# Kernel tuning notes

Measured on AMD Instinct MI355X. Metric: run time of the kernel, lower is better.

The kernel has to match this reference:

```python
import jax, jax.numpy as jnp
import numpy as np

H_KV = 8          # num_key_value_heads (hard-coded in module)
N_HEADS = 32
HEAD_DIM = 128
GROUPS = N_HEADS // H_KV
EPS = 1e-05
ROPE_THETA = 10000.0


def rotate_half(x):
    x1, x2 = jnp.split(x, 2, axis=-1)
    return jnp.concatenate((-x2, x1), axis=-1)


def rms_norm(x, w, eps=EPS):
    xf = x.astype(jnp.float32)
    var = jnp.mean(xf * xf, axis=-1, keepdims=True)
    return (w * (xf * jax.lax.rsqrt(var + eps))).astype(x.dtype)


def setup_inputs() -> dict:
    key = jax.random.key(0)
    k1, k2, k3 = jax.random.split(key, 3)
    B, S, D = 2, 2048, 4096
    hidden_states = jax.random.normal(k1, (B, S, D), dtype=jnp.float32)
    # RoPE tables (what custom_pos_emb carries)
    inv_freq = 1.0 / (ROPE_THETA ** (jnp.arange(0, HEAD_DIM, 2, dtype=jnp.float32) / HEAD_DIM))
    t = jnp.arange(S, dtype=jnp.float32)
    freqs = jnp.outer(t, inv_freq)                 # [S, HEAD_DIM/2]
    emb = jnp.concatenate((freqs, freqs), axis=-1)  # [S, HEAD_DIM]
    cos = jnp.cos(emb)[None]                        # [1, S, HEAD_DIM]
    sin = jnp.sin(emb)[None]
    w_qkv = jax.random.normal(k2, (6144, D), dtype=jnp.float32) * 0.02
    w_o = jax.random.normal(k3, (D, D), dtype=jnp.float32) * 0.02
    q_norm_w = jnp.ones((HEAD_DIM,), dtype=jnp.float32)
    k_norm_w = jnp.ones((HEAD_DIM,), dtype=jnp.float32)
    return {"hidden_states": hidden_states, "cos": cos, "sin": sin,
            "w_qkv": w_qkv, "w_o": w_o, "q_norm_w": q_norm_w, "k_norm_w": k_norm_w}


def reference(hidden_states, cos, sin, w_qkv, w_o, q_norm_w, k_norm_w):
    B, S, D = hidden_states.shape
    qkv = hidden_states @ w_qkv.T                                    # [B,S,6144]
    qkv = qkv.reshape(B, S, H_KV, GROUPS + 2, HEAD_DIM)
    q = qkv[:, :, :, :GROUPS]                                        # [B,S,Hkv,G,d]
    k = qkv[:, :, :, GROUPS]                                         # [B,S,Hkv,d]
    v = qkv[:, :, :, GROUPS + 1]                                     # [B,S,Hkv,d]
    # to [B, heads, S, d]
    q = q.reshape(B, S, N_HEADS, HEAD_DIM).transpose(0, 2, 1, 3)     # [B,Hq,S,d]
    k = k.transpose(0, 2, 1, 3)                                      # [B,Hkv,S,d]
    v = v.transpose(0, 2, 1, 3)
    # RoPE (cos/sin: [1,S,d] -> unsqueeze head dim)
    c = cos[:, None]  # [1,1,S,d]
    s = sin[:, None]
    q = q * c + rotate_half(q) * s
    k = k * c + rotate_half(k) * s
    # per-head RMSNorm
    q = rms_norm(q, q_norm_w)
    k = rms_norm(k, k_norm_w)
    # GQA attention without materializing repeated K/V
    qg = q.reshape(B, H_KV, GROUPS, S, HEAD_DIM)
    scale = 1.0 / np.sqrt(HEAD_DIM).astype(np.float32)
    scores = jnp.einsum('bkgqd,bksd->bkgqs', qg, k) * scale          # [B,Hkv,G,S,S]
    probs = jax.nn.softmax(scores, axis=-1)
    out = jnp.einsum('bkgqs,bksd->bkgqd', probs, v)                  # [B,Hkv,G,S,d]
    out = out.reshape(B, N_HEADS, S, HEAD_DIM).transpose(0, 2, 1, 3).reshape(B, S, D)
    return out @ w_o.T
```

## Files before the change

### kernel.cpp

```cpp
#include <hip/hip_runtime.h>
#include <hip/hip_bf16.h>

typedef __attribute__((ext_vector_type(8))) short short8;
typedef __attribute__((ext_vector_type(4))) float floatx4;

static __device__ __forceinline__ short bf16bits(float f) {
    __hip_bfloat16 h = __float2bfloat16(f);
    return __builtin_bit_cast(short, h);
}

#define GLDS(g, l) __builtin_amdgcn_global_load_lds( \
    (const __attribute__((address_space(1))) void*)(g), \
    (__attribute__((address_space(3))) void*)(l), 16, 0, 0)

__global__ __launch_bounds__(256) void cvt_bf16(
    const float* __restrict__ src, __hip_bfloat16* __restrict__ dst)
{
    size_t i = ((size_t)blockIdx.x * 256 + threadIdx.x) * 8;
    floatx4 f0 = *(const floatx4*)(src + i);
    floatx4 f1 = *(const floatx4*)(src + i + 4);
    short8 s;
#pragma unroll
    for (int j = 0; j < 4; j++) { s[j] = bf16bits(f0[j]); s[j + 4] = bf16bits(f1[j]); }
    *(short8*)((short*)dst + i) = s;
}

template<typename CT>
__global__ __launch_bounds__(256) void gemm_bt_fast(
    const __hip_bfloat16* __restrict__ A,
    const __hip_bfloat16* __restrict__ W,
    CT* __restrict__ C, int M, int N, int K)
{
    __shared__ alignas(16) short lA[128 * 64];
    __shared__ alignas(16) short lB[128 * 64];

    const int tid  = threadIdx.x;
    const int wave = tid >> 6;
    const int lane = tid & 63;
    const int quad = lane >> 4;
    const int l16  = lane & 15;

    const int m0 = blockIdx.x * 128;
    const int n0 = blockIdx.y * 128;
    const int wm = (wave & 1) * 64;
    const int wn = (wave >> 1) * 64;

    const int srow = lane >> 3;
    const int sblk = (lane & 7) ^ srow;
    const int scol = sblk * 8;

    const short* Ag = (const short*)A;
    const short* Wg = (const short*)W;

    floatx4 acc[4][4];
#pragma unroll
    for (int i = 0; i < 4; i++)
#pragma unroll
        for (int j = 0; j < 4; j++) acc[i][j] = (floatx4)0.0f;

    for (int k0 = 0; k0 < K; k0 += 64) {
        __syncthreads();
#pragma unroll
        for (int i = 0; i < 4; i++) {
            int c   = wave * 4 + i;
            int row = c * 8 + srow;
            GLDS(Ag + (size_t)(m0 + row) * K + k0 + scol, &lA[c * 512]);
            GLDS(Wg + (size_t)(n0 + row) * K + k0 + scol, &lB[c * 512]);
        }
        __syncthreads();
#pragma unroll
        for (int kk2 = 0; kk2 < 2; kk2++) {
            const int pb = ((kk2 * 4 + quad) ^ (l16 & 7)) * 8;
            short8 af[4], bf[4];
#pragma unroll
            for (int i = 0; i < 4; i++)
                af[i] = *(const short8*)(&lA[(wm + i * 16 + l16) * 64 + pb]);
#pragma unroll
            for (int j = 0; j < 4; j++)
                bf[j] = *(const short8*)(&lB[(wn + j * 16 + l16) * 64 + pb]);
#pragma unroll
            for (int i = 0; i < 4; i++)
#pragma unroll
                for (int j = 0; j < 4; j++)
                    acc[i][j] = __builtin_amdgcn_mfma_f32_16x16x32_bf16(
                        af[i], bf[j], acc[i][j], 0, 0, 0);
        }
    }
#pragma unroll
    for (int i = 0; i < 4; i++)
#pragma unroll
        for (int j = 0; j < 4; j++) {
            int gm = m0 + wm + i * 16 + quad * 4;
            int gn = n0 + wn + j * 16 + l16;
#pragma unroll
            for (int r = 0; r < 4; r++) {
                float v = acc[i][j][r];
                if constexpr (sizeof(CT) == 2)
                    C[(size_t)(gm + r) * N + gn] = (CT)__float2bfloat16(v);
                else
                    C[(size_t)(gm + r) * N + gn] = (CT)v;
            }
        }
}

template<bool AF32, typename CT>
__global__ __launch_bounds__(256) void gemm_bt_slow(
    const void* __restrict__ A,
    const float* __restrict__ Wf,
    CT* __restrict__ C, int M, int N, int K)
{
    __shared__ alignas(16) short lA[128 * 72];
    __shared__ alignas(16) short lB[128 * 72];

    const int tid  = threadIdx.x;
    const int wave = tid >> 6;
    const int lane = tid & 63;
    const int quad = lane >> 4;
    const int l16  = lane & 15;

    const int m0 = blockIdx.x * 128;
    const int n0 = blockIdx.y * 128;
    const int wm = (wave & 1) * 64;
    const int wn = (wave >> 1) * 64;

    floatx4 acc[4][4];
#pragma unroll
    for (int i = 0; i < 4; i++)
#pragma unroll
        for (int j = 0; j < 4; j++) acc[i][j] = (floatx4)0.0f;

    const short* Ab = (const short*)A;
    const float* Af = (const float*)A;

    for (int k0 = 0; k0 < K; k0 += 64) {
        __syncthreads();
#pragma unroll
        for (int i = 0; i < 4; i++) {
            int chunk = tid + i * 256;
            int row = chunk >> 3;
            int cc  = chunk & 7;
            if (AF32) {
                const float* src = Af + (size_t)(m0 + row) * K + k0 + cc * 8;
                floatx4 f0 = *(const floatx4*)(src);
                floatx4 f1 = *(const floatx4*)(src + 4);
                short8 s;
#pragma unroll
                for (int j = 0; j < 4; j++) { s[j] = bf16bits(f0[j]); s[j + 4] = bf16bits(f1[j]); }
                *(short8*)(&lA[row * 72 + cc * 8]) = s;
            } else {
                *(short8*)(&lA[row * 72 + cc * 8]) =
                    *(const short8*)(Ab + (size_t)(m0 + row) * K + k0 + cc * 8);
            }
            const float* src = Wf + (size_t)(n0 + row) * K + k0 + cc * 8;
            floatx4 f0 = *(const floatx4*)(src);
            floatx4 f1 = *(const floatx4*)(src + 4);
            short8 s;
#pragma unroll
            for (int j = 0; j < 4; j++) { s[j] = bf16bits(f0[j]); s[j + 4] = bf16bits(f1[j]); }
            *(short8*)(&lB[row * 72 + cc * 8]) = s;
        }
        __syncthreads();
#pragma unroll
        for (int kk = 0; kk < 64; kk += 32) {
            short8 af[4], bf[4];
#pragma unroll
            for (int i = 0; i < 4; i++)
                af[i] = *(const short8*)(&lA[(wm + i * 16 + l16) * 72 + kk + quad * 8]);
#pragma unroll
            for (int j = 0; j < 4; j++)
                bf[j] = *(const short8*)(&lB[(wn + j * 16 + l16) * 72 + kk + quad * 8]);
#pragma unroll
            for (int i = 0; i < 4; i++)
#pragma unroll
                for (int j = 0; j < 4; j++)
                    acc[i][j] = __builtin_amdgcn_mfma_f32_16x16x32_bf16(
                        af[i], bf[j], acc[i][j], 0, 0, 0);
        }
    }
#pragma unroll
    for (int i = 0; i < 4; i++)
#pragma unroll
        for (int j = 0; j < 4; j++) {
            int gm = m0 + wm + i * 16 + quad * 4;
            int gn = n0 + wn + j * 16 + l16;
#pragma unroll
            for (int r = 0; r < 4; r++) {
                float v = acc[i][j][r];
                if constexpr (sizeof(CT) == 2)
                    C[(size_t)(gm + r) * N + gn] = (CT)__float2bfloat16(v);
                else
                    C[(size_t)(gm + r) * N + gn] = (CT)v;
            }
        }
}

__global__ __launch_bounds__(256) void rope_norm(
    __hip_bfloat16* __restrict__ qkv,
    const float* __restrict__ cosb,
    const float* __restrict__ sinb,
    const float* __restrict__ qw,
    const float* __restrict__ kw)
{
    int wid  = blockIdx.x * 4 + (threadIdx.x >> 6);
    int lane = threadIdx.x & 63;
    int token = wid / 40;
    int idx   = wid % 40;
    int s = token & 2047;

    int off;
    const float* w;
    if (idx < 32) { off = (idx >> 2) * 768 + (idx & 3) * 128; w = qw; }
    else          { off = (idx - 32) * 768 + 512;             w = kw; }

    short* p = (short*)(qkv + (size_t)token * 6144 + off);
    int d = lane * 2;

    unsigned int pv = *(const unsigned int*)(p + d);
    float x0 = __builtin_bit_cast(float, pv << 16);
    float x1 = __builtin_bit_cast(float, pv & 0xffff0000u);

    float ox0 = __shfl_xor(x0, 32, 64);
    float ox1 = __shfl_xor(x1, 32, 64);

    float2 cv = *(const float2*)(cosb + s * 128 + d);
    float2 sv = *(const float2*)(sinb + s * 128 + d);
    float sgn = (lane < 32) ? -1.0f : 1.0f;
    float y0 = fmaf(sgn * ox0, sv.x, x0 * cv.x);
    float y1 = fmaf(sgn * ox1, sv.y, x1 * cv.y);

    float ss = y0 * y0 + y1 * y1;
#pragma unroll
    for (int m = 1; m < 64; m <<= 1) ss += __shfl_xor(ss, m, 64);
    float r = rsqrtf(ss * (1.0f / 128.0f) + 1e-5f);

    float2 wv = *(const float2*)(w + d);
    unsigned int out = (unsigned int)(unsigned short)bf16bits(y0 * r * wv.x)
                     | ((unsigned int)(unsigned short)bf16bits(y1 * r * wv.y) << 16);
    *(unsigned int*)(p + d) = out;
}

__global__ __launch_bounds__(256) void vtrans(
    const __hip_bfloat16* __restrict__ qkv, __hip_bfloat16* __restrict__ Vt)
{
    __shared__ alignas(16) short lT[64 * 136];

    const int bid   = blockIdx.x;
    const int stile = bid & 31;
    const int kvh   = (bid >> 5) & 7;
    const int b     = bid >> 8;
    const int tid   = threadIdx.x;
    const size_t voff = (size_t)kvh * 768 + 640;
    const short* qkvs = (const short*)qkv;

#pragma unroll
    for (int i = 0; i < 4; i++) {
        int chunk = tid + i * 256;
        int t  = chunk >> 4;
        int dc = chunk & 15;
        size_t tok = (size_t)(b * 2048 + stile * 64 + t);
        *(short8*)(&lT[t * 136 + dc * 8]) =
            *(const short8*)(qkvs + tok * 6144 + voff + dc * 8);
    }
    __syncthreads();

    int d  = tid >> 1;
    int kh = (tid & 1) * 32;
    short* out = (short*)Vt + ((size_t)((b * 8 + kvh) * 128 + d)) * 2048
               + stile * 64 + kh;
#pragma unroll
    for (int jb = 0; jb < 4; jb++) {
        short8 s;
#pragma unroll
        for (int j = 0; j < 8; j++) s[j] = lT[(kh + jb * 8 + j) * 136 + d];
        *(short8*)(out + jb * 8) = s;
    }
}

__global__ __launch_bounds__(256, 2) void attn_kernel(
    const __hip_bfloat16* __restrict__ qkv,
    const __hip_bfloat16* __restrict__ Vt,
    __hip_bfloat16* __restrict__ attn_out)
{
    __shared__ alignas(16) short lK[2][64 * 128];
    __shared__ alignas(16) short lVt[2][128 * 64];
    __shared__ alignas(16) short lP[4][32 * 64];

    const int bid0 = blockIdx.x;
    const int bid  = (bid0 & 7) * 128 + (bid0 >> 3);
    const int qt   = bid & 15;
    const int h    = (bid >> 4) & 31;
    const int b    = bid >> 9;
    const int kvh  = h >> 2;
    const int wave = threadIdx.x >> 6;
    const int lane = threadIdx.x & 63;
    const int quad = lane >> 4;
    const int l16  = lane & 15;

    const size_t qoff = (size_t)kvh * 768 + (size_t)(h & 3) * 128;
    const size_t koff = (size_t)kvh * 768 + 512;
    const short* qkvs = (const short*)qkv;
    const short* Vts  = (const short*)Vt + ((size_t)(b * 8 + kvh) * 128) * 2048;

    short8 qf[2][4];
#pragma unroll
    for (int t = 0; t < 2; t++) {
        const int qrow = qt * 128 + wave * 32 + t * 16 + l16;
        const size_t qtok = (size_t)(b * 2048 + qrow);
#pragma unroll
        for (int kk = 0; kk < 4; kk++)
            qf[t][kk] = *(const short8*)(qkvs + qtok * 6144 + qoff + kk * 32 + quad * 8);
    }

    floatx4 o[2][8];
#pragma unroll
    for (int t = 0; t < 2; t++)
#pragma unroll
        for (int n = 0; n < 8; n++) o[t][n] = (floatx4)0.0f;
    float mrow[2][4], lsum[2][4];
#pragma unroll
    for (int t = 0; t < 2; t++)
#pragma unroll
        for (int r = 0; r < 4; r++) { mrow[t][r] = -3.0e4f; lsum[t][r] = 0.0f; }

    const float scale2 = 0.08838834764831845f * 1.4426950408889634f;
    const float THR2   = 11.5418f;

    const int k_row = lane >> 4;
    const int v_row = lane >> 3;
    const int v_blk = (lane & 7) ^ v_row;

#pragma unroll
    for (int i = 0; i < 4; i++) {
        int c = wave * 4 + i;
        int k_blk = (lane & 15) ^ ((c * 4 + k_row) & 15);
        size_t tok = (size_t)(b * 2048 + c * 4 + k_row);
        GLDS(qkvs + tok * 6144 + koff + k_blk * 8, &lK[0][c * 512]);
        int d = c * 8 + v_row;
        GLDS(Vts + (size_t)d * 2048 + v_blk * 8, &lVt[0][c * 512]);
    }

    int cur = 0;
    for (int kt = 0; kt < 32; kt++) {
        __syncthreads();

        if (kt < 31) {
            short* nK = &lK[cur ^ 1][0];
            short* nV = &lVt[cur ^ 1][0];
#pragma unroll
            for (int i = 0; i < 4; i++) {
                int c = wave * 4 + i;
                int k_blk = (lane & 15) ^ ((c * 4 + k_row) & 15);
                size_t tok = (size_t)(b * 2048 + (kt + 1) * 64 + c * 4 + k_row);
                GLDS(qkvs + tok * 6144 + koff + k_blk * 8, nK + c * 512);
                int d = c * 8 + v_row;
                GLDS(Vts + (size_t)d * 2048 + (kt + 1) * 64 + v_blk * 8, nV + c * 512);
            }
        }

        const short* lKc = &lK[cur][0];
        const short* lVc = &lVt[cur][0];

        floatx4 sc[2][4];
#pragma unroll
        for (int t = 0; t < 2; t++)
#pragma unroll
            for (int n = 0; n < 4; n++) sc[t][n] = (floatx4)0.0f;
#pragma unroll
        for (int kk = 0; kk < 4; kk++) {
#pragma unroll
            for (int n = 0; n < 4; n++) {
                short8 bfr = *(const short8*)(
                    &lKc[(n * 16 + l16) * 128 + (((kk * 4 + quad) ^ l16)) * 8]);
                sc[0][n] = __builtin_amdgcn_mfma_f32_16x16x32_bf16(qf[0][kk], bfr, sc[0][n], 0, 0, 0);
                sc[1][n] = __builtin_amdgcn_mfma_f32_16x16x32_bf16(qf[1][kk], bfr, sc[1][n], 0, 0, 0);
            }
        }

#pragma unroll
        for (int t = 0; t < 2; t++) {
            float mx[4]; int grow = 0;
#pragma unroll
            for (int r = 0; r < 4; r++) {
                float m0 = fmaxf(fmaxf(sc[t][0][r], sc[t][1][r]),
                                 fmaxf(sc[t][2][r], sc[t][3][r])) * scale2;
#pragma unroll
                for (int m = 1; m < 16; m <<= 1) m0 = fmaxf(m0, __shfl_xor(m0, m, 64));
                mx[r] = m0;
                grow |= (m0 > mrow[t][r] + THR2) ? 1 : 0;
            }
            const bool big = __any(grow) != 0;
            float alpha[4];
            if (big) {
#pragma unroll
                for (int r = 0; r < 4; r++) {
                    float mn = fmaxf(mrow[t][r], mx[r]);
                    alpha[r] = exp2f(mrow[t][r] - mn);
                    mrow[t][r] = mn;
                }
            }
#pragma unroll
            for (int n = 0; n < 4; n++)
#pragma unroll
                for (int r = 0; r < 4; r++) {
                    float p = exp2f(sc[t][n][r] * scale2 - mrow[t][r]);
                    sc[t][n][r] = p;
                    int row = t * 16 + quad * 4 + r;
                    int pblk = (n * 2 + (l16 >> 3)) ^ (row & 7);
                    lP[wave][row * 64 + pblk * 8 + (l16 & 7)] = bf16bits(p);
                }
#pragma unroll
            for (int r = 0; r < 4; r++) {
                float ps = (sc[t][0][r] + sc[t][1][r]) + (sc[t][2][r] + sc[t][3][r]);
                if (big) lsum[t][r] = lsum[t][r] * alpha[r] + ps;
                else     lsum[t][r] += ps;
            }
            if (big) {
#pragma unroll
                for (int n = 0; n < 8; n++)
#pragma unroll
                    for (int r = 0; r < 4; r++) o[t][n][r] *= alpha[r];
            }
        }

        __threadfence_block();

#pragma unroll
        for (int kk2 = 0; kk2 < 2; kk2++) {
            const int pb = ((kk2 * 4 + quad) ^ (l16 & 7)) * 8;
            short8 pf0 = *(const short8*)(&lP[wave][(l16)      * 64 + pb]);
            short8 pf1 = *(const short8*)(&lP[wave][(16 + l16) * 64 + pb]);
#pragma unroll
            for (int n = 0; n < 8; n++) {
                short8 vf = *(const short8*)(&lVc[(n * 16 + l16) * 64 + pb]);
                o[0][n] = __builtin_amdgcn_mfma_f32_16x16x32_bf16(pf0, vf, o[0][n], 0, 0, 0);
                o[1][n] = __builtin_amdgcn_mfma_f32_16x16x32_bf16(pf1, vf, o[1][n], 0, 0, 0);
            }
        }

        cur ^= 1;
    }

#pragma unroll
    for (int t = 0; t < 2; t++)
#pragma unroll
        for (int r = 0; r < 4; r++) {
            float s = lsum[t][r];
#pragma unroll
            for (int m = 1; m < 16; m <<= 1) s += __shfl_xor(s, m, 64);
            lsum[t][r] = 1.0f / s;
        }

#pragma unroll
    for (int t = 0; t < 2; t++)
#pragma unroll
        for (int n = 0; n < 8; n++)
#pragma unroll
            for (int r = 0; r < 4; r++) {
                int row = qt * 128 + wave * 32 + t * 16 + quad * 4 + r;
                size_t tok = (size_t)(b * 2048 + row);
                attn_out[tok * 4096 + h * 128 + n * 16 + l16] =
                    __float2bfloat16(o[t][n][r] * lsum[t][r]);
            }
}

extern "C" void kernel_launch(void* const* d_in, const int* in_sizes, int n_in,
                              void* d_out, int out_size, void* d_ws, size_t ws_size,
                              hipStream_t stream) {
    const float* hidden = (const float*)d_in[0];
    const float* cosb   = (const float*)d_in[1];
    const float* sinb   = (const float*)d_in[2];
    const float* w_qkv  = (const float*)d_in[3];
    const float* w_o    = (const float*)d_in[4];
    const float* qw     = (const float*)d_in[5];
    const float* kw     = (const float*)d_in[6];

    char* ws = (char*)d_ws;
    __hip_bfloat16* qkv    = (__hip_bfloat16*)ws;
    __hip_bfloat16* attn_o = (__hip_bfloat16*)(ws + 50331648);
    __hip_bfloat16* hb  = (__hip_bfloat16*)(ws + 83886080);
    __hip_bfloat16* wb1 = (__hip_bfloat16*)(ws + 117440512);
    __hip_bfloat16* wb2 = (__hip_bfloat16*)(ws + 167772160);
    const size_t WS_FAST = 201326592;

    __hip_bfloat16* Vt = (__hip_bfloat16*)d_out;
    float* outp        = (float*)d_out;

    const bool fast = (ws_size >= WS_FAST);

    if (fast) {
        cvt_bf16<<<16777216 / 8 / 256, 256, 0, stream>>>(hidden, hb);
        cvt_bf16<<<25165824 / 8 / 256, 256, 0, stream>>>(w_qkv, wb1);
        cvt_bf16<<<16777216 / 8 / 256, 256, 0, stream>>>(w_o, wb2);
        dim3 g1(32, 48);
        gemm_bt_fast<__hip_bfloat16><<<g1, 256, 0, stream>>>(hb, wb1, qkv, 4096, 6144, 4096);
    } else {
        dim3 g1(32, 48);
        gemm_bt_slow<true, __hip_bfloat16><<<g1, 256, 0, stream>>>(hidden, w_qkv, qkv, 4096, 6144, 4096);
    }

    rope_norm<<<40960, 256, 0, stream>>>(qkv, cosb, sinb, qw, kw);

    vtrans<<<512, 256, 0, stream>>>(qkv, Vt);

    attn_kernel<<<1024, 256, 0, stream>>>(qkv, Vt, attn_o);

    dim3 g2(32, 32);
    if (fast) {
        gemm_bt_fast<float><<<g2, 256, 0, stream>>>(attn_o, wb2, outp, 4096, 4096, 4096);
    } else {
        gemm_bt_slow<false, float><<<g2, 256, 0, stream>>>(attn_o, w_o, outp, 4096, 4096, 4096);
    }
}
```

Measured before the change: 894.2 us.

## Compute transposed S in attention to keep P in registers instead of LDS

Swaps the MFMA operands so each lane holds scores for one query row across keys. Row max and sum then need only two cross-lane shuffles, and the online-softmax state shrinks to one value per tile. Probabilities are packed to bf16 with v_cvt_pk_bf16_f32 and rearranged with lane shuffles into the PV operand layout, removing the per-wave LDS buffer, its scalar stores and the block fence. Output stores become 4-element vector writes. The cost is extra ds_bpermute shuffles and selects, plus inline asm that depends on the ISA providing that instruction.

New measurement: 875.7 us. 1.02x faster.

```diff
diff --git a/kernel.cpp b/kernel.cpp
--- a/kernel.cpp
+++ b/kernel.cpp
@@ -2,11 +2,19 @@
 #include <hip/hip_bf16.h>
 
 typedef __attribute__((ext_vector_type(8))) short short8;
+typedef __attribute__((ext_vector_type(4))) short short4v;
 typedef __attribute__((ext_vector_type(4))) float floatx4;
+typedef __attribute__((ext_vector_type(4))) unsigned int uintx4;
 
 static __device__ __forceinline__ short bf16bits(float f) {
     __hip_bfloat16 h = __float2bfloat16(f);
     return __builtin_bit_cast(short, h);
+}
+
+static __device__ __forceinline__ unsigned int cvtpk(float lo, float hi) {
+    unsigned int r;
+    asm("v_cvt_pk_bf16_f32 %0, %1, %2" : "=v"(r) : "v"(lo), "v"(hi));
+    return r;
 }
 
 #define GLDS(g, l) __builtin_amdgcn_global_load_lds( \
@@ -283,7 +291,6 @@
 {
     __shared__ alignas(16) short lK[2][64 * 128];
     __shared__ alignas(16) short lVt[2][128 * 64];
-    __shared__ alignas(16) short lP[4][32 * 64];
 
     const int bid0 = blockIdx.x;
     const int bid  = (bid0 & 7) * 128 + (bid0 >> 3);
@@ -291,8 +298,8 @@
     const int h    = (bid >> 4) & 31;
     const int b    = bid >> 9;
     const int kvh  = h >> 2;
+    const int lane = threadIdx.x & 63;
     const int wave = threadIdx.x >> 6;
-    const int lane = threadIdx.x & 63;
     const int quad = lane >> 4;
     const int l16  = lane & 15;
 
@@ -316,11 +323,8 @@
     for (int t = 0; t < 2; t++)
 #pragma unroll
         for (int n = 0; n < 8; n++) o[t][n] = (floatx4)0.0f;
-    float mrow[2][4], lsum[2][4];
-#pragma unroll
-    for (int t = 0; t < 2; t++)
-#pragma unroll
-        for (int r = 0; r < 4; r++) { mrow[t][r] = -3.0e4f; lsum[t][r] = 0.0f; }
+    float mrow[2] = { -3.0e4f, -3.0e4f };
+    float lsum[2] = { 0.0f, 0.0f };
 
     const float scale2 = 0.08838834764831845f * 1.4426950408889634f;
     const float THR2   = 11.5418f;
@@ -328,6 +332,10 @@
     const int k_row = lane >> 4;
     const int v_row = lane >> 3;
     const int v_blk = (lane & 7) ^ v_row;
+
+    const int srcA = l16 + ((lane & 16) << 1);
+    const int srcB = srcA + 16;
+    const bool hi2 = (quad >> 1) != 0;
 
 #pragma unroll
     for (int i = 0; i < 4; i++) {
@@ -369,98 +377,108 @@
         for (int kk = 0; kk < 4; kk++) {
 #pragma unroll
             for (int n = 0; n < 4; n++) {
-                short8 bfr = *(const short8*)(
+                short8 kf = *(const short8*)(
                     &lKc[(n * 16 + l16) * 128 + (((kk * 4 + quad) ^ l16)) * 8]);
-                sc[0][n] = __builtin_amdgcn_mfma_f32_16x16x32_bf16(qf[0][kk], bfr, sc[0][n], 0, 0, 0);
-                sc[1][n] = __builtin_amdgcn_mfma_f32_16x16x32_bf16(qf[1][kk], bfr, sc[1][n], 0, 0, 0);
-            }
-        }
-
+                sc[0][n] = __builtin_amdgcn_mfma_f32_16x16x32_bf16(kf, qf[0][kk], sc[0][n], 0, 0, 0);
+                sc[1][n] = __builtin_amdgcn_mfma_f32_16x16x32_bf16(kf, qf[1][kk], sc[1][n], 0, 0, 0);
+            }
+        }
+
+        short8 pb[2][2];
 #pragma unroll
         for (int t = 0; t < 2; t++) {
-            float mx[4]; int grow = 0;
-#pragma unroll
-            for (int r = 0; r < 4; r++) {
-                float m0 = fmaxf(fmaxf(sc[t][0][r], sc[t][1][r]),
-                                 fmaxf(sc[t][2][r], sc[t][3][r])) * scale2;
-#pragma unroll
-                for (int m = 1; m < 16; m <<= 1) m0 = fmaxf(m0, __shfl_xor(m0, m, 64));
-                mx[r] = m0;
-                grow |= (m0 > mrow[t][r] + THR2) ? 1 : 0;
-            }
-            const bool big = __any(grow) != 0;
-            float alpha[4];
-            if (big) {
+            float ma = fmaxf(fmaxf(sc[t][0][0], sc[t][0][1]), fmaxf(sc[t][0][2], sc[t][0][3]));
+            float mb = fmaxf(fmaxf(sc[t][1][0], sc[t][1][1]), fmaxf(sc[t][1][2], sc[t][1][3]));
+            float mc = fmaxf(fmaxf(sc[t][2][0], sc[t][2][1]), fmaxf(sc[t][2][2], sc[t][2][3]));
+            float md = fmaxf(fmaxf(sc[t][3][0], sc[t][3][1]), fmaxf(sc[t][3][2], sc[t][3][3]));
+            float mr = fmaxf(fmaxf(ma, mb), fmaxf(mc, md));
+            mr = fmaxf(mr, __shfl_xor(mr, 16, 64));
+            mr = fmaxf(mr, __shfl_xor(mr, 32, 64));
+            float mx = mr * scale2;
+
+            int grown = mx > mrow[t] + THR2;
+            if (__any(grown)) {
+                float mn = fmaxf(mrow[t], mx);
+                float alpha = exp2f(mrow[t] - mn);
+                mrow[t] = mn;
+                lsum[t] *= alpha;
+#pragma unroll
+                for (int n = 0; n < 8; n++)
+#pragma unroll
+                    for (int r = 0; r < 4; r++) o[t][n][r] *= alpha;
+            }
+
+            const float nm = -mrow[t];
+            float ps = 0.0f;
+            unsigned int pk[4][2];
+#pragma unroll
+            for (int n = 0; n < 4; n++) {
 #pragma unroll
                 for (int r = 0; r < 4; r++) {
-                    float mn = fmaxf(mrow[t][r], mx[r]);
-                    alpha[r] = exp2f(mrow[t][r] - mn);
-                    mrow[t][r] = mn;
+                    float pv = exp2f(fmaf(sc[t][n][r], scale2, nm));
+                    sc[t][n][r] = pv;
+                    ps += pv;
                 }
-            }
-#pragma unroll
-            for (int n = 0; n < 4; n++)
-#pragma unroll
-                for (int r = 0; r < 4; r++) {
-                    float p = exp2f(sc[t][n][r] * scale2 - mrow[t][r]);
-                    sc[t][n][r] = p;
-                    int row = t * 16 + quad * 4 + r;
-                    int pblk = (n * 2 + (l16 >> 3)) ^ (row & 7);
-                    lP[wave][row * 64 + pblk * 8 + (l16 & 7)] = bf16bits(p);
-                }
-#pragma unroll
-            for (int r = 0; r < 4; r++) {
-                float ps = (sc[t][0][r] + sc[t][1][r]) + (sc[t][2][r] + sc[t][3][r]);
-                if (big) lsum[t][r] = lsum[t][r] * alpha[r] + ps;
-                else     lsum[t][r] += ps;
-            }
-            if (big) {
-#pragma unroll
-                for (int n = 0; n < 8; n++)
-#pragma unroll
-                    for (int r = 0; r < 4; r++) o[t][n][r] *= alpha[r];
-            }
-        }
-
-        __threadfence_block();
+                pk[n][0] = cvtpk(sc[t][n][0], sc[t][n][1]);
+                pk[n][1] = cvtpk(sc[t][n][2], sc[t][n][3]);
+            }
+            lsum[t] += ps;
+
+#pragma unroll
+            for (int kk2 = 0; kk2 < 2; kk2++) {
+                unsigned int a0 = __shfl(pk[2 * kk2][0],     srcA, 64);
+                unsigned int a1 = __shfl(pk[2 * kk2 + 1][0], srcA, 64);
+                unsigned int a2 = __shfl(pk[2 * kk2][1],     srcA, 64);
+                unsigned int a3 = __shfl(pk[2 * kk2 + 1][1], srcA, 64);
+                unsigned int c0 = __shfl(pk[2 * kk2][0],     srcB, 64);
+                unsigned int c1 = __shfl(pk[2 * kk2 + 1][0], srcB, 64);
+                unsigned int c2 = __shfl(pk[2 * kk2][1],     srcB, 64);
+                unsigned int c3 = __shfl(pk[2 * kk2 + 1][1], srcB, 64);
+                uintx4 u;
+                u[0] = hi2 ? a1 : a0;
+                u[1] = hi2 ? a3 : a2;
+                u[2] = hi2 ? c1 : c0;
+                u[3] = hi2 ? c3 : c2;
+                pb[t][kk2] = __builtin_bit_cast(short8, u);
+            }
+        }
 
 #pragma unroll
         for (int kk2 = 0; kk2 < 2; kk2++) {
-            const int pb = ((kk2 * 4 + quad) ^ (l16 & 7)) * 8;
-            short8 pf0 = *(const short8*)(&lP[wave][(l16)      * 64 + pb]);
-            short8 pf1 = *(const short8*)(&lP[wave][(16 + l16) * 64 + pb]);
+            const int pbv = ((kk2 * 4 + quad) ^ (l16 & 7)) * 8;
 #pragma unroll
             for (int n = 0; n < 8; n++) {
-                short8 vf = *(const short8*)(&lVc[(n * 16 + l16) * 64 + pb]);
-                o[0][n] = __builtin_amdgcn_mfma_f32_16x16x32_bf16(pf0, vf, o[0][n], 0, 0, 0);
-                o[1][n] = __builtin_amdgcn_mfma_f32_16x16x32_bf16(pf1, vf, o[1][n], 0, 0, 0);
+                short8 vf = *(const short8*)(&lVc[(n * 16 + l16) * 64 + pbv]);
+                o[0][n] = __builtin_amdgcn_mfma_f32_16x16x32_bf16(vf, pb[0][kk2], o[0][n], 0, 0, 0);
+                o[1][n] = __builtin_amdgcn_mfma_f32_16x16x32_bf16(vf, pb[1][kk2], o[1][n], 0, 0, 0);
             }
         }
 
         cur ^= 1;
     }
 
-#pragma unroll
-    for (int t = 0; t < 2; t++)
-#pragma unroll
-        for (int r = 0; r < 4; r++) {
-            float s = lsum[t][r];
-#pragma unroll
-            for (int m = 1; m < 16; m <<= 1) s += __shfl_xor(s, m, 64);
-            lsum[t][r] = 1.0f / s;
-        }
-
-#pragma unroll
-    for (int t = 0; t < 2; t++)
-#pragma unroll
-        for (int n = 0; n < 8; n++)
-#pragma unroll
-            for (int r = 0; r < 4; r++) {
-                int row = qt * 128 + wave * 32 + t * 16 + quad * 4 + r;
-                size_t tok = (size_t)(b * 2048 + row);
-                attn_out[tok * 4096 + h * 128 + n * 16 + l16] =
-                    __float2bfloat16(o[t][n][r] * lsum[t][r]);
-            }
+    float inv[2];
+#pragma unroll
+    for (int t = 0; t < 2; t++) {
+        float s = lsum[t];
+        s += __shfl_xor(s, 16, 64);
+        s += __shfl_xor(s, 32, 64);
+        inv[t] = 1.0f / s;
+    }
+
+#pragma unroll
+    for (int t = 0; t < 2; t++) {
+        const int row = qt * 128 + wave * 32 + t * 16 + l16;
+        const size_t tok = (size_t)(b * 2048 + row);
+        short* outp = (short*)attn_out + tok * 4096 + h * 128 + quad * 4;
+#pragma unroll
+        for (int n = 0; n < 8; n++) {
+            short4v s4;
+#pragma unroll
+            for (int r = 0; r < 4; r++) s4[r] = bf16bits(o[t][n][r] * inv[t]);
+            *(short4v*)(outp + n * 16) = s4;
+        }
+    }
 }
 
 extern "C" void kernel_launch(void* const* d_in, const int* in_sizes, int n_in,
```
